# Optimization experiments

Measured on AMD Instinct MI355X. Metric: run time of the kernel, lower is better.

## Reference

```python
import jax, jax.numpy as jnp
import numpy as np

N_EXPERTS = 9
MODEL_DIM = 256
NUM_HEADS = 4
N_TOKENS = 4096
LN_EPS = 1e-5


def setup_inputs() -> dict:
    key0 = jax.random.key(0)
    ks = jax.random.split(key0, 8)
    D, E = MODEL_DIM, N_EXPERTS
    x = jax.random.normal(ks[0], (N_TOKENS, D), dtype=jnp.float32)
    label = jax.random.randint(ks[1], (N_TOKENS,), 0, E, dtype=jnp.int64)
    s = 0.02
    Wq = jax.random.normal(ks[2], (E, D, D), dtype=jnp.float32) * s
    Wk = jax.random.normal(ks[3], (E, D, D), dtype=jnp.float32) * s
    Wv = jax.random.normal(ks[4], (E, D, D), dtype=jnp.float32) * s
    bq = jnp.zeros((E, D), dtype=jnp.float32)
    bk = jnp.zeros((E, D), dtype=jnp.float32)
    bv = jnp.zeros((E, D), dtype=jnp.float32)
    Wf = jax.random.normal(ks[5], (D, D), dtype=jnp.float32) * s
    bf = jnp.zeros((D,), dtype=jnp.float32)
    gamma = jnp.ones((D,), dtype=jnp.float32)
    beta = jnp.zeros((D,), dtype=jnp.float32)
    return {"x": x, "label": label, "Wq": Wq, "bq": bq, "Wk": Wk, "bk": bk,
            "Wv": Wv, "bv": bv, "Wf": Wf, "bf": bf, "gamma": gamma, "beta": beta}


def reference(x, label, Wq, bq, Wk, bk, Wv, bv, Wf, bf, gamma, beta):
    # v2 path: per-label expert QKV projection + within-label self-attention.
    N, D = x.shape
    H = NUM_HEADS
    dph = D // H  # dim_per_head = 64
    # NOTE: source uses scale = (dim_per_head // num_heads) ** -0.5
    scale = float((dph // H)) ** -0.5
    idx = jnp.arange(N)
    lbl = label.astype(jnp.int32)

    # Compute all 9 expert projections, then select per-token (dense dispatch).
    q = jnp.einsum('nd,edh->enh', x, Wq)[lbl, idx] + bq[lbl]  # [N, D]
    k = jnp.einsum('nd,edh->enh', x, Wk)[lbl, idx] + bk[lbl]
    v = jnp.einsum('nd,edh->enh', x, Wv)[lbl, idx] + bv[lbl]

    qh = q.reshape(N, H, dph)
    kh = k.reshape(N, H, dph)
    vh = v.reshape(N, H, dph)

    # Attention restricted to tokens with the same label (equivalent to the
    # per-label gather -> bmm -> scatter in the torch loop).
    scores = jnp.einsum('nhd,mhd->hnm', qh, kh) * scale  # [H, N, N]
    same = (lbl[:, None] == lbl[None, :])  # [N, N]
    scores = jnp.where(same[None, :, :], scores, -jnp.inf)
    attn = jax.nn.softmax(scores, axis=-1)
    ctx = jnp.einsum('hnm,mhd->nhd', attn, vh).reshape(N, D)

    out = ctx @ Wf + bf
    h = x + out  # residual is the (gathered) original key
    mean = jnp.mean(h, axis=-1, keepdims=True)
    var = jnp.mean(jnp.square(h - mean), axis=-1, keepdims=True)
    return gamma * (h - mean) / jnp.sqrt(var + LN_EPS) + beta
```

## Files before the change

kernel.cpp:

```cpp
#include <hip/hip_runtime.h>
#include <math.h>

#define N_TOK 4096
#define DIM 256
#define NHEAD 4
#define DPH 64
#define NEXP 9
#define SCALE 0.25f
#define TQ 16
#define MAXST 80
#define GPAD 4736
#define VPITCH 4736

typedef short s8 __attribute__((ext_vector_type(8)));
typedef short s4 __attribute__((ext_vector_type(4)));
typedef float f4 __attribute__((ext_vector_type(4)));

static __device__ __forceinline__ short f2bf(float f) {
  union { float f; unsigned u; } v;
  v.f = f;
  unsigned r = (v.u + 0x7FFFu + ((v.u >> 16) & 1u)) >> 16;
  return (short)r;
}

static __device__ __forceinline__ float wave_sum(float v) {
#pragma unroll
  for (int o = 32; o > 0; o >>= 1) v += __shfl_xor(v, o, 64);
  return v;
}

__global__ void k_build(const int* __restrict__ label, int* __restrict__ perm,
                        int* __restrict__ gs, int* __restrict__ gep,
                        int* __restrict__ st_e, int* __restrict__ st_row,
                        int* __restrict__ nstp) {
  __shared__ int cnt[NEXP];
  __shared__ int base[NEXP];
  int tid = threadIdx.x;
  if (tid < NEXP) cnt[tid] = 0;
  __syncthreads();
  for (int t = tid; t < N_TOK; t += 256) atomicAdd(&cnt[label[t]], 1);
  __syncthreads();
  if (tid == 0) {
    int run = 0, ns = 0;
    for (int e = 0; e < NEXP; e++) {
      gs[e] = run;
      base[e] = run;
      int end = run + cnt[e];
      gep[e] = end;
      for (int r = run; r < end; r += 64) { st_e[ns] = e; st_row[ns] = r; ns++; }
      run = (end + 63) & ~63;
    }
    *nstp = ns;
  }
  __syncthreads();
  for (int t = tid; t < N_TOK; t += 256) {
    int e = label[t];
    int pos = atomicAdd(&base[e], 1);
    perm[pos] = t;
  }
}

__global__ __launch_bounds__(256) void k_castx(const float* __restrict__ x,
                                               const int* __restrict__ perm,
                                               const int* __restrict__ gs,
                                               const int* __restrict__ gep,
                                               short* __restrict__ xb) {
  int grow = blockIdx.x * 64 + (threadIdx.x >> 2);
  int qd = (threadIdx.x & 3) * 64;
  bool valid = false;
#pragma unroll
  for (int e = 0; e < NEXP; e++) valid |= (grow >= gs[e] && grow < gep[e]);
  short* dst = xb + (size_t)grow * DIM + qd;
  if (valid) {
    const float* src = x + (size_t)perm[grow] * DIM + qd;
#pragma unroll
    for (int i = 0; i < 16; i++) {
      float4 v = *(const float4*)(src + i * 4);
      s4 o;
      o[0] = f2bf(v.x); o[1] = f2bf(v.y); o[2] = f2bf(v.z); o[3] = f2bf(v.w);
      *(s4*)(dst + i * 4) = o;
    }
  } else {
#pragma unroll
    for (int i = 0; i < 16; i++) *(s4*)(dst + i * 4) = (s4){0, 0, 0, 0};
  }
}

__global__ __launch_bounds__(256) void k_castw(const float* __restrict__ Wq,
                                               const float* __restrict__ Wk,
                                               const float* __restrict__ Wv,
                                               const float* __restrict__ Wf,
                                               short* __restrict__ WbT) {
  __shared__ short tile[64 * 68];
  int slab = blockIdx.y;
  const float* src;
  if (slab < 9) src = Wq + (size_t)slab * 65536;
  else if (slab < 18) src = Wk + (size_t)(slab - 9) * 65536;
  else if (slab < 27) src = Wv + (size_t)(slab - 18) * 65536;
  else src = Wf;
  int d0 = (blockIdx.x >> 2) * 64, h0 = (blockIdx.x & 3) * 64;
  int tid = threadIdx.x;
  int rl = tid >> 4;
  int hh = (tid & 15) * 4;
#pragma unroll
  for (int p = 0; p < 4; p++) {
    int dl = p * 16 + rl;
    float4 v = *(const float4*)(src + (size_t)(d0 + dl) * 256 + h0 + hh);
    s4 o;
    o[0] = f2bf(v.x); o[1] = f2bf(v.y); o[2] = f2bf(v.z); o[3] = f2bf(v.w);
    *(s4*)&tile[dl * 68 + hh] = o;
  }
  __syncthreads();
  int h = tid >> 2, dq = (tid & 3) * 16;
  s8 pa, pb;
#pragma unroll
  for (int i = 0; i < 8; i++) {
    pa[i] = tile[(dq + i) * 68 + h];
    pb[i] = tile[(dq + 8 + i) * 68 + h];
  }
  short* dst = WbT + (size_t)slab * 65536 + (size_t)(h0 + h) * 256 + d0 + dq;
  *(s8*)dst = pa;
  *(s8*)(dst + 8) = pb;
}

__global__ __launch_bounds__(256) void k_proj(
    const short* __restrict__ xb, const short* __restrict__ WbT,
    const float* __restrict__ bq, const float* __restrict__ bk,
    const float* __restrict__ bv, const int* __restrict__ st_e,
    const int* __restrict__ st_row, const int* __restrict__ nstp,
    short* __restrict__ qg, short* __restrict__ kg, short* __restrict__ vgT) {
  int b = blockIdx.x;
  if (b >= *nstp) return;
  int gy = blockIdx.y;
  int mtx = blockIdx.z;
  int e = st_e[b];
  int row0 = st_row[b];
  int tid = threadIdx.x, wl = tid >> 6, lane = tid & 63;
  int m = lane & 15, quad = lane >> 4;

  const short* A = xb + (size_t)(row0 + wl * 16 + m) * DIM;
  const short* B = WbT + (size_t)(mtx * 9 + e) * 65536;
  const float* bias = (mtx == 0) ? bq : (mtx == 1) ? bk : bv;

  f4 acc[4];
#pragma unroll
  for (int t = 0; t < 4; t++) acc[t] = (f4){0.f, 0.f, 0.f, 0.f};

#pragma unroll
  for (int kc = 0; kc < 8; kc++) {
    s8 a = *(const s8*)(A + kc * 32 + quad * 8);
#pragma unroll
    for (int t = 0; t < 4; t++) {
      s8 wb = *(const s8*)(B + (size_t)(gy * 64 + t * 16 + m) * 256 + kc * 32 +
                           quad * 8);
      acc[t] = __builtin_amdgcn_mfma_f32_16x16x32_bf16(a, wb, acc[t], 0, 0, 0);
    }
  }

#pragma unroll
  for (int t = 0; t < 4; t++) {
    int col = gy * 64 + t * 16 + m;
    float bs = bias[e * DIM + col];
#pragma unroll
    for (int r = 0; r < 4; r++) {
      int grow = row0 + wl * 16 + quad * 4 + r;
      short o = f2bf(acc[t][r] + bs);
      if (mtx == 2) vgT[(size_t)col * VPITCH + grow] = o;
      else if (mtx == 1) kg[(size_t)grow * DIM + col] = o;
      else qg[(size_t)grow * DIM + col] = o;
    }
  }
}

__global__ __launch_bounds__(256) void k_attn(
    const short* __restrict__ qg, const short* __restrict__ kg,
    const short* __restrict__ vgT, const int* __restrict__ perm,
    const int* __restrict__ gs, const int* __restrict__ gep,
    const int* __restrict__ st_e, const int* __restrict__ st_row,
    const int* __restrict__ nstp, short* __restrict__ cb) {
  int b = blockIdx.x;
  if (b >= *nstp) return;
  int h = blockIdx.y;
  int e = st_e[b];
  int row0 = st_row[b];
  int g0 = gs[e], kend = gep[e];

  int tid = threadIdx.x;
  int wl = tid >> 6;
  int lane = tid & 63;
  int m = lane & 15;
  int quad = lane >> 4;

  __shared__ short k_s[64 * 72];
  __shared__ short v_s[64 * 72];
  __shared__ short p_s[4 * 16 * 72];

  int qrow = row0 + wl * 16 + m;
  if (qrow >= kend) qrow = row0;
  s8 qf0 = *(const s8*)&qg[(size_t)qrow * DIM + h * DPH + quad * 8];
  s8 qf1 = *(const s8*)&qg[(size_t)qrow * DIM + h * DPH + 32 + quad * 8];

  f4 o_acc[4];
  float m_i[4], l_i[4];
#pragma unroll
  for (int t = 0; t < 4; t++) o_acc[t] = (f4){0.f, 0.f, 0.f, 0.f};
#pragma unroll
  for (int r = 0; r < 4; r++) { m_i[r] = -INFINITY; l_i[r] = 0.f; }

  for (int jt = g0; jt < kend; jt += 64) {
    __syncthreads();
#pragma unroll
    for (int it = 0; it < 2; it++) {
      int id = it * 256 + tid;
      int row = id >> 3, cc = id & 7;
      s8 kv = *(const s8*)&kg[(size_t)(jt + row) * DIM + h * DPH + cc * 8];
      *(s8*)&k_s[row * 72 + cc * 8] = kv;
      s8 vv = *(const s8*)&vgT[(size_t)(h * DPH + row) * VPITCH + jt + cc * 8];
      *(s8*)&v_s[row * 72 + cc * 8] = vv;
    }
    __syncthreads();

    f4 s_acc[4];
#pragma unroll
    for (int t = 0; t < 4; t++) s_acc[t] = (f4){0.f, 0.f, 0.f, 0.f};
#pragma unroll
    for (int t = 0; t < 4; t++) {
      s8 kb0 = *(s8*)&k_s[(t * 16 + m) * 72 + quad * 8];
      s8 kb1 = *(s8*)&k_s[(t * 16 + m) * 72 + 32 + quad * 8];
      s_acc[t] = __builtin_amdgcn_mfma_f32_16x16x32_bf16(qf0, kb0, s_acc[t], 0, 0, 0);
      s_acc[t] = __builtin_amdgcn_mfma_f32_16x16x32_bf16(qf1, kb1, s_acc[t], 0, 0, 0);
    }

    float cf[4];
#pragma unroll
    for (int r = 0; r < 4; r++) {
      float sv[4];
      float mx = -INFINITY;
#pragma unroll
      for (int t = 0; t < 4; t++) {
        float xv = s_acc[t][r] * SCALE;
        if (jt + t * 16 + m >= kend) xv = -INFINITY;
        sv[t] = xv;
        mx = fmaxf(mx, xv);
      }
#pragma unroll
      for (int o = 8; o > 0; o >>= 1) mx = fmaxf(mx, __shfl_xor(mx, o, 64));
      float c = __expf(m_i[r] - fmaxf(m_i[r], mx));
      float mnew = fmaxf(m_i[r], mx);
      float ls = 0.f;
#pragma unroll
      for (int t = 0; t < 4; t++) {
        float p = __expf(sv[t] - mnew);
        ls += p;
        p_s[(wl * 16 + quad * 4 + r) * 72 + t * 16 + m] = f2bf(p);
      }
#pragma unroll
      for (int o = 8; o > 0; o >>= 1) ls += __shfl_xor(ls, o, 64);
      l_i[r] = l_i[r] * c + ls;
      m_i[r] = mnew;
      cf[r] = c;
    }

#pragma unroll
    for (int t = 0; t < 4; t++)
#pragma unroll
      for (int r = 0; r < 4; r++) o_acc[t][r] *= cf[r];

#pragma unroll
    for (int kk = 0; kk < 2; kk++) {
      s8 pa = *(s8*)&p_s[(wl * 16 + m) * 72 + kk * 32 + quad * 8];
#pragma unroll
      for (int t = 0; t < 4; t++) {
        s8 vb = *(s8*)&v_s[(t * 16 + m) * 72 + kk * 32 + quad * 8];
        o_acc[t] = __builtin_amdgcn_mfma_f32_16x16x32_bf16(pa, vb, o_acc[t], 0, 0, 0);
      }
    }
  }

#pragma unroll
  for (int r = 0; r < 4; r++) {
    int qr = row0 + wl * 16 + quad * 4 + r;
    if (qr < kend) {
      int tok = perm[qr];
      float inv = 1.f / l_i[r];
#pragma unroll
      for (int t = 0; t < 4; t++)
        cb[(size_t)tok * DIM + h * DPH + t * 16 + m] = f2bf(o_acc[t][r] * inv);
    }
  }
}

__global__ __launch_bounds__(256) void k_out(
    const short* __restrict__ cb, const short* __restrict__ WbT,
    const float* __restrict__ x, const float* __restrict__ bfv,
    const float* __restrict__ gamma, const float* __restrict__ beta,
    float* __restrict__ out) {
  int t0 = blockIdx.x * TQ;
  int tid = threadIdx.x, wl = tid >> 6, lane = tid & 63;
  int m = lane & 15, quad = lane >> 4;
  __shared__ float h_s[TQ * 260];

  const short* A = cb + (size_t)(t0 + m) * DIM;
  const short* B = WbT + (size_t)27 * 65536;

  f4 acc[4];
#pragma unroll
  for (int t = 0; t < 4; t++) acc[t] = (f4){0.f, 0.f, 0.f, 0.f};

#pragma unroll
  for (int kc = 0; kc < 8; kc++) {
    s8 a = *(const s8*)(A + kc * 32 + quad * 8);
#pragma unroll
    for (int t = 0; t < 4; t++) {
      s8 wb = *(const s8*)(B + (size_t)(wl * 64 + t * 16 + m) * 256 + kc * 32 +
                           quad * 8);
      acc[t] = __builtin_amdgcn_mfma_f32_16x16x32_bf16(a, wb, acc[t], 0, 0, 0);
    }
  }

#pragma unroll
  for (int t = 0; t < 4; t++) {
    int col = wl * 64 + t * 16 + m;
    float bs = bfv[col];
#pragma unroll
    for (int r = 0; r < 4; r++) h_s[(quad * 4 + r) * 260 + col] = acc[t][r] + bs;
  }
  __syncthreads();

  int w = tid >> 6;
#pragma unroll
  for (int rr = 0; rr < 4; rr++) {
    int row = w * 4 + rr;
    float hv[4];
#pragma unroll
    for (int k2 = 0; k2 < 4; k2++)
      hv[k2] = h_s[row * 260 + lane + 64 * k2] +
               x[(size_t)(t0 + row) * DIM + lane + 64 * k2];
    float sum = hv[0] + hv[1] + hv[2] + hv[3];
    float mean = wave_sum(sum) * (1.f / 256.f);
    float sq = 0.f;
#pragma unroll
    for (int k2 = 0; k2 < 4; k2++) {
      float dd = hv[k2] - mean;
      sq += dd * dd;
    }
    float var = wave_sum(sq) * (1.f / 256.f);
    float rstd = rsqrtf(var + 1e-5f);
#pragma unroll
    for (int k2 = 0; k2 < 4; k2++) {
      int c = lane + 64 * k2;
      out[(size_t)(t0 + row) * DIM + c] =
          gamma[c] * ((hv[k2] - mean) * rstd) + beta[c];
    }
  }
}

extern "C" void kernel_launch(void* const* d_in, const int* in_sizes, int n_in,
                              void* d_out, int out_size, void* d_ws,
                              size_t ws_size, hipStream_t stream) {
  const float* x = (const float*)d_in[0];
  const int* label = (const int*)d_in[1];
  const float* Wq = (const float*)d_in[2];
  const float* bq = (const float*)d_in[3];
  const float* Wk = (const float*)d_in[4];
  const float* bk = (const float*)d_in[5];
  const float* Wv = (const float*)d_in[6];
  const float* bv = (const float*)d_in[7];
  const float* Wf = (const float*)d_in[8];
  const float* bfv = (const float*)d_in[9];
  const float* gamma = (const float*)d_in[10];
  const float* beta = (const float*)d_in[11];
  float* out = (float*)d_out;

  int* perm = (int*)d_ws;
  int* gs = perm + 8192;
  int* gep = gs + 16;
  int* st_e = gep + 16;
  int* st_row = st_e + 128;
  int* nstp = st_row + 128;
  short* qg = (short*)((char*)d_ws + 65536);
  short* kg = qg + (size_t)GPAD * DIM;
  short* vgT = kg + (size_t)GPAD * DIM;
  short* WbT = vgT + (size_t)DIM * VPITCH;
  short* xb = WbT + (size_t)28 * 65536;
  short* cb = xb;

  hipLaunchKernelGGL(k_build, dim3(1), dim3(256), 0, stream, label, perm, gs,
                     gep, st_e, st_row, nstp);
  hipLaunchKernelGGL(k_castw, dim3(16, 28), dim3(256), 0, stream, Wq, Wk, Wv,
                     Wf, WbT);
  hipLaunchKernelGGL(k_castx, dim3(GPAD / 64), dim3(256), 0, stream, x, perm,
                     gs, gep, xb);
  hipLaunchKernelGGL(k_proj, dim3(MAXST, 4, 3), dim3(256), 0, stream, xb, WbT,
                     bq, bk, bv, st_e, st_row, nstp, qg, kg, vgT);
  hipLaunchKernelGGL(k_attn, dim3(MAXST, NHEAD), dim3(256), 0, stream, qg, kg,
                     vgT, perm, gs, gep, st_e, st_row, nstp, cb);
  hipLaunchKernelGGL(k_out, dim3(N_TOK / TQ), dim3(256), 0, stream, cb, WbT, x,
                     bfv, gamma, beta, out);
}
```

Before: 154.1 us.

## Prefetch K/V tiles and GEMM operands, drop online-softmax max, gather context via iperm

```diff
diff --git a/kernel.cpp b/kernel.cpp
--- a/kernel.cpp
+++ b/kernel.cpp
@@ -30,9 +30,9 @@
 }
 
 __global__ void k_build(const int* __restrict__ label, int* __restrict__ perm,
-                        int* __restrict__ gs, int* __restrict__ gep,
-                        int* __restrict__ st_e, int* __restrict__ st_row,
-                        int* __restrict__ nstp) {
+                        int* __restrict__ iperm, int* __restrict__ gs,
+                        int* __restrict__ gep, int* __restrict__ st_e,
+                        int* __restrict__ st_row, int* __restrict__ nstp) {
   __shared__ int cnt[NEXP];
   __shared__ int base[NEXP];
   int tid = threadIdx.x;
@@ -57,6 +57,7 @@
     int e = label[t];
     int pos = atomicAdd(&base[e], 1);
     perm[pos] = t;
+    iperm[t] = pos;
   }
 }
 
@@ -138,23 +139,36 @@
   int tid = threadIdx.x, wl = tid >> 6, lane = tid & 63;
   int m = lane & 15, quad = lane >> 4;
 
-  const short* A = xb + (size_t)(row0 + wl * 16 + m) * DIM;
-  const short* B = WbT + (size_t)(mtx * 9 + e) * 65536;
+  const short* Ap = xb + (size_t)(row0 + wl * 16 + m) * DIM + quad * 8;
+  const short* Bp = WbT + (size_t)(mtx * 9 + e) * 65536 +
+                    (size_t)(gy * 64 + m) * 256 + quad * 8;
   const float* bias = (mtx == 0) ? bq : (mtx == 1) ? bk : bv;
 
+  s8 ac = *(const s8*)Ap;
+  s8 bc[4];
+#pragma unroll
+  for (int t = 0; t < 4; t++) bc[t] = *(const s8*)(Bp + t * 16 * 256);
+
   f4 acc[4];
 #pragma unroll
   for (int t = 0; t < 4; t++) acc[t] = (f4){0.f, 0.f, 0.f, 0.f};
 
 #pragma unroll
   for (int kc = 0; kc < 8; kc++) {
-    s8 a = *(const s8*)(A + kc * 32 + quad * 8);
-#pragma unroll
-    for (int t = 0; t < 4; t++) {
-      s8 wb = *(const s8*)(B + (size_t)(gy * 64 + t * 16 + m) * 256 + kc * 32 +
-                           quad * 8);
-      acc[t] = __builtin_amdgcn_mfma_f32_16x16x32_bf16(a, wb, acc[t], 0, 0, 0);
-    }
+    s8 an = ac;
+    s8 bn[4] = {bc[0], bc[1], bc[2], bc[3]};
+    if (kc < 7) {
+      an = *(const s8*)(Ap + (kc + 1) * 32);
+#pragma unroll
+      for (int t = 0; t < 4; t++)
+        bn[t] = *(const s8*)(Bp + t * 16 * 256 + (kc + 1) * 32);
+    }
+#pragma unroll
+    for (int t = 0; t < 4; t++)
+      acc[t] = __builtin_amdgcn_mfma_f32_16x16x32_bf16(ac, bc[t], acc[t], 0, 0, 0);
+    ac = an;
+#pragma unroll
+    for (int t = 0; t < 4; t++) bc[t] = bn[t];
   }
 
 #pragma unroll
@@ -174,10 +188,10 @@
 
 __global__ __launch_bounds__(256) void k_attn(
     const short* __restrict__ qg, const short* __restrict__ kg,
-    const short* __restrict__ vgT, const int* __restrict__ perm,
-    const int* __restrict__ gs, const int* __restrict__ gep,
-    const int* __restrict__ st_e, const int* __restrict__ st_row,
-    const int* __restrict__ nstp, short* __restrict__ cb) {
+    const short* __restrict__ vgT, const int* __restrict__ gs,
+    const int* __restrict__ gep, const int* __restrict__ st_e,
+    const int* __restrict__ st_row, const int* __restrict__ nstp,
+    short* __restrict__ cg) {
   int b = blockIdx.x;
   if (b >= *nstp) return;
   int h = blockIdx.y;
@@ -190,6 +204,8 @@
   int lane = tid & 63;
   int m = lane & 15;
   int quad = lane >> 4;
+  int r0 = tid >> 3;
+  int c0 = (tid & 7) * 8;
 
   __shared__ short k_s[64 * 72];
   __shared__ short v_s[64 * 72];
@@ -201,23 +217,30 @@
   s8 qf1 = *(const s8*)&qg[(size_t)qrow * DIM + h * DPH + 32 + quad * 8];
 
   f4 o_acc[4];
-  float m_i[4], l_i[4];
+  float l_r[4];
 #pragma unroll
   for (int t = 0; t < 4; t++) o_acc[t] = (f4){0.f, 0.f, 0.f, 0.f};
 #pragma unroll
-  for (int r = 0; r < 4; r++) { m_i[r] = -INFINITY; l_i[r] = 0.f; }
-
+  for (int r = 0; r < 4; r++) l_r[r] = 0.f;
+
+  s8 pk0, pk1, pv0, pv1;
+#define PREF(JT)                                                            \
+  do {                                                                      \
+    pk0 = *(const s8*)&kg[(size_t)((JT) + r0) * DIM + h * DPH + c0];        \
+    pk1 = *(const s8*)&kg[(size_t)((JT) + r0 + 32) * DIM + h * DPH + c0];   \
+    pv0 = *(const s8*)&vgT[(size_t)(h * DPH + r0) * VPITCH + (JT) + c0];    \
+    pv1 = *(const s8*)&vgT[(size_t)(h * DPH + r0 + 32) * VPITCH + (JT) + c0]; \
+  } while (0)
+
+  PREF(g0);
   for (int jt = g0; jt < kend; jt += 64) {
     __syncthreads();
-#pragma unroll
-    for (int it = 0; it < 2; it++) {
-      int id = it * 256 + tid;
-      int row = id >> 3, cc = id & 7;
-      s8 kv = *(const s8*)&kg[(size_t)(jt + row) * DIM + h * DPH + cc * 8];
-      *(s8*)&k_s[row * 72 + cc * 8] = kv;
-      s8 vv = *(const s8*)&vgT[(size_t)(h * DPH + row) * VPITCH + jt + cc * 8];
-      *(s8*)&v_s[row * 72 + cc * 8] = vv;
-    }
+    *(s8*)&k_s[r0 * 72 + c0] = pk0;
+    *(s8*)&k_s[(r0 + 32) * 72 + c0] = pk1;
+    *(s8*)&v_s[r0 * 72 + c0] = pv0;
+    *(s8*)&v_s[(r0 + 32) * 72 + c0] = pv1;
+    int jn = jt + 64;
+    if (jn < kend) PREF(jn);
     __syncthreads();
 
     f4 s_acc[4];
@@ -231,40 +254,16 @@
       s_acc[t] = __builtin_amdgcn_mfma_f32_16x16x32_bf16(qf1, kb1, s_acc[t], 0, 0, 0);
     }
 
-    float cf[4];
-#pragma unroll
-    for (int r = 0; r < 4; r++) {
-      float sv[4];
-      float mx = -INFINITY;
-#pragma unroll
-      for (int t = 0; t < 4; t++) {
-        float xv = s_acc[t][r] * SCALE;
-        if (jt + t * 16 + m >= kend) xv = -INFINITY;
-        sv[t] = xv;
-        mx = fmaxf(mx, xv);
-      }
-#pragma unroll
-      for (int o = 8; o > 0; o >>= 1) mx = fmaxf(mx, __shfl_xor(mx, o, 64));
-      float c = __expf(m_i[r] - fmaxf(m_i[r], mx));
-      float mnew = fmaxf(m_i[r], mx);
-      float ls = 0.f;
-#pragma unroll
-      for (int t = 0; t < 4; t++) {
-        float p = __expf(sv[t] - mnew);
-        ls += p;
+#pragma unroll
+    for (int t = 0; t < 4; t++) {
+      bool ok = (jt + t * 16 + m) < kend;
+#pragma unroll
+      for (int r = 0; r < 4; r++) {
+        float p = ok ? __expf(s_acc[t][r] * SCALE) : 0.f;
+        l_r[r] += p;
         p_s[(wl * 16 + quad * 4 + r) * 72 + t * 16 + m] = f2bf(p);
       }
-#pragma unroll
-      for (int o = 8; o > 0; o >>= 1) ls += __shfl_xor(ls, o, 64);
-      l_i[r] = l_i[r] * c + ls;
-      m_i[r] = mnew;
-      cf[r] = c;
-    }
-
-#pragma unroll
-    for (int t = 0; t < 4; t++)
-#pragma unroll
-      for (int r = 0; r < 4; r++) o_acc[t][r] *= cf[r];
+    }
 
 #pragma unroll
     for (int kk = 0; kk < 2; kk++) {
@@ -276,32 +275,38 @@
       }
     }
   }
+#undef PREF
 
 #pragma unroll
   for (int r = 0; r < 4; r++) {
-    int qr = row0 + wl * 16 + quad * 4 + r;
-    if (qr < kend) {
-      int tok = perm[qr];
-      float inv = 1.f / l_i[r];
-#pragma unroll
-      for (int t = 0; t < 4; t++)
-        cb[(size_t)tok * DIM + h * DPH + t * 16 + m] = f2bf(o_acc[t][r] * inv);
-    }
+    float lt = l_r[r];
+#pragma unroll
+    for (int o = 8; o > 0; o >>= 1) lt += __shfl_xor(lt, o, 64);
+    float inv = 1.f / lt;
+    int grow = row0 + wl * 16 + quad * 4 + r;
+#pragma unroll
+    for (int t = 0; t < 4; t++)
+      cg[(size_t)grow * DIM + h * DPH + t * 16 + m] = f2bf(o_acc[t][r] * inv);
   }
 }
 
 __global__ __launch_bounds__(256) void k_out(
-    const short* __restrict__ cb, const short* __restrict__ WbT,
+    const short* __restrict__ cg, const short* __restrict__ WbT,
     const float* __restrict__ x, const float* __restrict__ bfv,
     const float* __restrict__ gamma, const float* __restrict__ beta,
-    float* __restrict__ out) {
+    const int* __restrict__ iperm, float* __restrict__ out) {
   int t0 = blockIdx.x * TQ;
   int tid = threadIdx.x, wl = tid >> 6, lane = tid & 63;
   int m = lane & 15, quad = lane >> 4;
   __shared__ float h_s[TQ * 260];
 
-  const short* A = cb + (size_t)(t0 + m) * DIM;
-  const short* B = WbT + (size_t)27 * 65536;
+  const short* Ap = cg + (size_t)iperm[t0 + m] * DIM + quad * 8;
+  const short* Bp = WbT + (size_t)27 * 65536 + (size_t)(wl * 64 + m) * 256 + quad * 8;
+
+  s8 ac = *(const s8*)Ap;
+  s8 bc[4];
+#pragma unroll
+  for (int t = 0; t < 4; t++) bc[t] = *(const s8*)(Bp + t * 16 * 256);
 
   f4 acc[4];
 #pragma unroll
@@ -309,13 +314,20 @@
 
 #pragma unroll
   for (int kc = 0; kc < 8; kc++) {
-    s8 a = *(const s8*)(A + kc * 32 + quad * 8);
-#pragma unroll
-    for (int t = 0; t < 4; t++) {
-      s8 wb = *(const s8*)(B + (size_t)(wl * 64 + t * 16 + m) * 256 + kc * 32 +
-                           quad * 8);
-      acc[t] = __builtin_amdgcn_mfma_f32_16x16x32_bf16(a, wb, acc[t], 0, 0, 0);
-    }
+    s8 an = ac;
+    s8 bn[4] = {bc[0], bc[1], bc[2], bc[3]};
+    if (kc < 7) {
+      an = *(const s8*)(Ap + (kc + 1) * 32);
+#pragma unroll
+      for (int t = 0; t < 4; t++)
+        bn[t] = *(const s8*)(Bp + t * 16 * 256 + (kc + 1) * 32);
+    }
+#pragma unroll
+    for (int t = 0; t < 4; t++)
+      acc[t] = __builtin_amdgcn_mfma_f32_16x16x32_bf16(ac, bc[t], acc[t], 0, 0, 0);
+    ac = an;
+#pragma unroll
+    for (int t = 0; t < 4; t++) bc[t] = bn[t];
   }
 
 #pragma unroll
@@ -373,7 +385,8 @@
   float* out = (float*)d_out;
 
   int* perm = (int*)d_ws;
-  int* gs = perm + 8192;
+  int* iperm = perm + 8192;
+  int* gs = iperm + 4096;
   int* gep = gs + 16;
   int* st_e = gep + 16;
   int* st_row = st_e + 128;
@@ -383,10 +396,10 @@
   short* vgT = kg + (size_t)GPAD * DIM;
   short* WbT = vgT + (size_t)DIM * VPITCH;
   short* xb = WbT + (size_t)28 * 65536;
-  short* cb = xb;
-
-  hipLaunchKernelGGL(k_build, dim3(1), dim3(256), 0, stream, label, perm, gs,
-                     gep, st_e, st_row, nstp);
+  short* cg = xb;
+
+  hipLaunchKernelGGL(k_build, dim3(1), dim3(256), 0, stream, label, perm,
+                     iperm, gs, gep, st_e, st_row, nstp);
   hipLaunchKernelGGL(k_castw, dim3(16, 28), dim3(256), 0, stream, Wq, Wk, Wv,
                      Wf, WbT);
   hipLaunchKernelGGL(k_castx, dim3(GPAD / 64), dim3(256), 0, stream, x, perm,
@@ -394,7 +407,7 @@
   hipLaunchKernelGGL(k_proj, dim3(MAXST, 4, 3), dim3(256), 0, stream, xb, WbT,
                      bq, bk, bv, st_e, st_row, nstp, qg, kg, vgT);
   hipLaunchKernelGGL(k_attn, dim3(MAXST, NHEAD), dim3(256), 0, stream, qg, kg,
-                     vgT, perm, gs, gep, st_e, st_row, nstp, cb);
-  hipLaunchKernelGGL(k_out, dim3(N_TOK / TQ), dim3(256), 0, stream, cb, WbT, x,
-                     bfv, gamma, beta, out);
-}
+                     vgT, gs, gep, st_e, st_row, nstp, cg);
+  hipLaunchKernelGGL(k_out, dim3(N_TOK / TQ), dim3(256), 0, stream, cg, WbT, x,
+                     bfv, gamma, beta, iperm, out);
+}
```

Result: faster. 147.6 us (-4.2%).
